# Performance work log

Measured on AMD Instinct MI355X. Metric: run time of the kernel, lower is better.

Reference implementation:

```python
import jax, jax.numpy as jnp
import numpy as np

STRIDE = 1
PAD = 1
K = 3  # kernel is asserted 3x3 in the original module


def _conv2d(x, w, b):
    out = jax.lax.conv_general_dilated(
        x, w, (STRIDE, STRIDE), [(PAD, PAD), (PAD, PAD)],
        dimension_numbers=("NCHW", "OIHW", "NCHW"))
    return out + b[None, :, None, None]


def _bilinear_sample(img, py, px):
    # img: [C, H, W]; py, px: [9, Ho, Wo] float sampling coords.
    # Zero-padded bilinear sampling (matches torchvision deform_conv2d).
    H, W = img.shape[1], img.shape[2]
    y0f = jnp.floor(py)
    x0f = jnp.floor(px)
    ly = py - y0f
    lx = px - x0f
    y0 = y0f.astype(jnp.int32)
    x0 = x0f.astype(jnp.int32)

    def g(yi, xi):
        valid = ((yi >= 0) & (yi < H) & (xi >= 0) & (xi < W)).astype(img.dtype)
        v = img[:, jnp.clip(yi, 0, H - 1), jnp.clip(xi, 0, W - 1)]  # [C,9,Ho,Wo]
        return v * valid[None]

    v00 = g(y0, x0)
    v01 = g(y0, x0 + 1)
    v10 = g(y0 + 1, x0)
    v11 = g(y0 + 1, x0 + 1)
    return (v00 * (1 - ly) * (1 - lx) + v01 * (1 - ly) * lx
            + v10 * ly * (1 - lx) + v11 * ly * lx)  # [C,9,Ho,Wo]


def setup_inputs() -> dict:
    key = jax.random.key(0)
    k1, k2, k3, k4 = jax.random.split(key, 4)
    B, C_in, C_out, H, W = 8, 64, 64, 128, 128
    x = jax.random.normal(k1, (B, C_in, H, W), dtype=jnp.float32)
    # offset predictor params (zero-init in original; small random here so
    # offsets are non-trivial, ~1-2 px)
    offset_w = jax.random.normal(k2, (4, C_in, K, K), dtype=jnp.float32) * 0.05
    offset_b = jax.random.normal(k3, (4,), dtype=jnp.float32) * 0.05
    weight = jax.random.normal(k4, (C_out, C_in, K, K), dtype=jnp.float32)
    return {"x": x, "offset_w": offset_w, "offset_b": offset_b, "weight": weight}


def reference(x, offset_w, offset_b, weight):
    B, C, H, W = x.shape
    o = _conv2d(x, offset_w, offset_b)  # [B, 4, Ho, Wo]
    o_t, o_b, o_l, o_r = o[:, 0], o[:, 1], o[:, 2], o[:, 3]
    z = jnp.zeros_like(o_t)
    # Original builds offset = cat([o_t,0,o_b]*3, [o_l]*3,[0]*3,[o_r]*3) (18 ch)
    # and torchvision reads interleaved (dy_k, dx_k) = (ch[2k], ch[2k+1]).
    # Faithful literal per-kernel-point offsets:
    dy = jnp.stack([o_t, o_b, z, o_t, o_b, o_l, z, z, o_r], axis=1)  # [B,9,Ho,Wo]
    dx = jnp.stack([z, o_t, o_b, z, o_l, o_l, z, o_r, o_r], axis=1)  # [B,9,Ho,Wo]
    Ho, Wo = o.shape[2], o.shape[3]
    ki = jnp.arange(9) // 3
    kj = jnp.arange(9) % 3
    base_y = (jnp.arange(Ho)[None, :, None] * STRIDE - PAD + ki[:, None, None])  # [9,Ho,1]
    base_x = (jnp.arange(Wo)[None, None, :] * STRIDE - PAD + kj[:, None, None])  # [9,1,Wo]
    py = base_y.astype(x.dtype) + dy  # [B,9,Ho,Wo]
    px = base_x.astype(x.dtype) + dx
    sampled = jax.vmap(_bilinear_sample)(x, py, px)  # [B,C,9,Ho,Wo]
    out = jnp.einsum("bckhw,ock->bohw", sampled,
                     weight.reshape(weight.shape[0], C, 9))
    return out
```

## Files before the change

kernel.cpp:

```cpp
#include <hip/hip_runtime.h>

#define H_   128
#define W_   128
#define CIN  64
#define COUT 64
#define B_   8
#define HW_  (H_*W_)

typedef __attribute__((ext_vector_type(8))) short  short8;
typedef __attribute__((ext_vector_type(8))) __bf16 bf16x8;
typedef __attribute__((ext_vector_type(4))) float  f32x4;

__device__ __forceinline__ ushort bf16r(float f) {
    uint u = __builtin_bit_cast(uint, f);
    u += 0x7fff + ((u >> 16) & 1);
    return (ushort)(u >> 16);
}

__global__ void prep_kernel(const float* __restrict__ wt, const float* __restrict__ ow,
                            float* __restrict__ owT, ushort* __restrict__ wTT2)
{
    int idx = blockIdx.x * 256 + threadIdx.x;
    if (idx < 9 * 64 * 64) {
        int kk = idx >> 12;
        int r  = idx & 4095;
        int co = r >> 6, c = r & 63;
        wTT2[idx] = bf16r(wt[(co * 64 + c) * 9 + kk]);
    }
    if (idx < 576 * 4) {
        int ck = idx >> 2, j = idx & 3;
        owT[idx] = ow[j * 576 + ck];
    }
}

__global__ __launch_bounds__(128) void offsets_kernel(
    const float* __restrict__ x, const float* __restrict__ owT,
    const float* __restrict__ ob, float* __restrict__ o)
{
    __shared__ float xs[16][3][132];

    int tid = threadIdx.x;
    int blk = blockIdx.x;
    int b = blk >> 7, h = blk & 127;
    int w = tid;

    for (int i = tid; i < 16 * 3; i += 128) {
        int c = i / 3, r = i - c * 3;
        xs[c][r][0] = 0.f; xs[c][r][1] = 0.f;
        xs[c][r][130] = 0.f; xs[c][r][131] = 0.f;
    }

    float a0 = 0.f, a1 = 0.f, a2 = 0.f, a3 = 0.f;
    const float4* owT4 = (const float4*)owT;

    for (int cc = 0; cc < 4; ++cc) {
        __syncthreads();
        for (int idx = tid; idx < 16 * 3 * 128; idx += 128) {
            int c_l = idx / 384;
            int rem = idx - c_l * 384;
            int row = rem >> 7, ww = rem & 127;
            int gy = h - 1 + row;
            float v = 0.f;
            if ((unsigned)gy < (unsigned)H_)
                v = x[((size_t)(b * CIN + cc * 16 + c_l) * H_ + gy) * W_ + ww];
            xs[c_l][row][ww + 2] = v;
        }
        __syncthreads();
        #pragma unroll
        for (int c_l = 0; c_l < 16; ++c_l) {
            int ckb = (cc * 16 + c_l) * 9;
            #pragma unroll
            for (int ki = 0; ki < 3; ++ki) {
                #pragma unroll
                for (int kj = 0; kj < 3; ++kj) {
                    float v = xs[c_l][ki][w + kj + 1];
                    float4 wv = owT4[ckb + ki * 3 + kj];
                    a0 += v * wv.x; a1 += v * wv.y;
                    a2 += v * wv.z; a3 += v * wv.w;
                }
            }
        }
    }

    size_t base = ((size_t)(b * 4) * H_ + h) * W_ + w;
    o[base]           = a0 + ob[0];
    o[base + HW_]     = a1 + ob[1];
    o[base + 2 * HW_] = a2 + ob[2];
    o[base + 3 * HW_] = a3 + ob[3];
}

__global__ __launch_bounds__(128) void main_kernel(
    const float* __restrict__ x, const float* __restrict__ o,
    const ushort* __restrict__ wTT2, float* __restrict__ out)
{
    __shared__ ushort a_lds[128][72];
    __shared__ ushort w_lds[64][72];

    int tid  = threadIdx.x;
    int blk  = blockIdx.x;
    int b    = blk >> 7, h = blk & 127;
    int w    = tid;
    int lane = tid & 63, wid = tid >> 6;

    size_t obase = ((size_t)(b * 4) * H_ + h) * W_ + w;
    float t  = o[obase];
    float bo = o[obase + HW_];
    float l_ = o[obase + 2 * HW_];
    float r_ = o[obase + 3 * HW_];

    const float* xb = x + ((size_t)b * CIN * HW_);

    f32x4 zero4 = {0.f, 0.f, 0.f, 0.f};
    f32x4 acc[4][4];
    #pragma unroll
    for (int i = 0; i < 4; ++i)
        #pragma unroll
        for (int j = 0; j < 4; ++j) acc[i][j] = zero4;

    for (int cc = 0; cc < 9; ++cc) {
        float dy, dx;
        switch (cc) {
            case 0: dy = t;   dx = 0.f; break;
            case 1: dy = bo;  dx = t;   break;
            case 2: dy = 0.f; dx = bo;  break;
            case 3: dy = t;   dx = 0.f; break;
            case 4: dy = bo;  dx = l_;  break;
            case 5: dy = l_;  dx = l_;  break;
            case 6: dy = 0.f; dx = 0.f; break;
            case 7: dy = 0.f; dx = r_;  break;
            default: dy = r_; dx = r_;  break;
        }
        int ki = cc / 3, kj = cc - ki * 3;
        float py  = (float)(h - 1 + ki) + dy;
        float pxf = (float)(w - 1 + kj) + dx;
        float y0f = floorf(py), x0f = floorf(pxf);
        float ly = py - y0f, lx = pxf - x0f;
        int y0 = (int)y0f, x0 = (int)x0f;
        int y1 = y0 + 1,   x1 = x0 + 1;
        bool vy0 = ((unsigned)y0 < (unsigned)H_);
        bool vy1 = ((unsigned)y1 < (unsigned)H_);
        bool vx0 = ((unsigned)x0 < (unsigned)W_);
        bool vx1 = ((unsigned)x1 < (unsigned)W_);
        int y0c = min(max(y0, 0), H_ - 1), y1c = min(max(y1, 0), H_ - 1);
        int x0c = min(max(x0, 0), W_ - 1), x1c = min(max(x1, 0), W_ - 1);
        int ia0 = y0c * W_ + x0c, ia1 = y0c * W_ + x1c;
        int ia2 = y1c * W_ + x0c, ia3 = y1c * W_ + x1c;
        float omly = 1.f - ly, omlx = 1.f - lx;
        float wt0 = (vy0 && vx0) ? omly * omlx : 0.f;
        float wt1 = (vy0 && vx1) ? omly * lx   : 0.f;
        float wt2 = (vy1 && vx0) ? ly * omlx   : 0.f;
        float wt3 = (vy1 && vx1) ? ly * lx     : 0.f;

        #pragma unroll
        for (int c8 = 0; c8 < 8; ++c8) {
            uint pk[4];
            #pragma unroll
            for (int i2 = 0; i2 < 4; ++i2) {
                const float* xc0 = xb + ((size_t)(c8 * 8 + i2 * 2) << 14);
                const float* xc1 = xb + ((size_t)(c8 * 8 + i2 * 2 + 1) << 14);
                float s0 = wt0 * xc0[ia0] + wt1 * xc0[ia1]
                         + wt2 * xc0[ia2] + wt3 * xc0[ia3];
                float s1 = wt0 * xc1[ia0] + wt1 * xc1[ia1]
                         + wt2 * xc1[ia2] + wt3 * xc1[ia3];
                pk[i2] = (uint)bf16r(s0) | ((uint)bf16r(s1) << 16);
            }
            *(uint4*)&a_lds[tid][c8 * 8] = make_uint4(pk[0], pk[1], pk[2], pk[3]);
        }

        {
            const uint4* src = (const uint4*)(wTT2 + cc * 4096);
            #pragma unroll
            for (int q = 0; q < 4; ++q) {
                int idx = tid + q * 128;
                int co = idx >> 3, c0 = (idx & 7) * 8;
                *(uint4*)&w_lds[co][c0] = src[idx];
            }
        }
        __syncthreads();

        #pragma unroll
        for (int s = 0; s < 2; ++s) {
            int krow = s * 32 + (lane >> 4) * 8;
            bf16x8 af[4];
            #pragma unroll
            for (int i = 0; i < 4; ++i)
                af[i] = __builtin_bit_cast(bf16x8,
                    *(const short8*)&a_lds[wid * 64 + i * 16 + (lane & 15)][krow]);
            #pragma unroll
            for (int j = 0; j < 4; ++j) {
                bf16x8 bf = __builtin_bit_cast(bf16x8,
                    *(const short8*)&w_lds[j * 16 + (lane & 15)][krow]);
                #pragma unroll
                for (int i = 0; i < 4; ++i)
                    acc[i][j] = __builtin_amdgcn_mfma_f32_16x16x32_bf16(
                        af[i], bf, acc[i][j], 0, 0, 0);
            }
        }
        __syncthreads();
    }

    #pragma unroll
    for (int i = 0; i < 4; ++i) {
        int pr = wid * 64 + i * 16 + (lane >> 4) * 4;
        #pragma unroll
        for (int j = 0; j < 4; ++j) {
            int co = j * 16 + (lane & 15);
            *(float4*)&out[((size_t)(b * COUT + co) * H_ + h) * W_ + pr] =
                *(float4*)&acc[i][j];
        }
    }
}

extern "C" void kernel_launch(void* const* d_in, const int* in_sizes, int n_in,
                              void* d_out, int out_size, void* d_ws, size_t ws_size,
                              hipStream_t stream)
{
    const float* x  = (const float*)d_in[0];
    const float* ow = (const float*)d_in[1];
    const float* ob = (const float*)d_in[2];
    const float* wt = (const float*)d_in[3];
    float* out = (float*)d_out;

    float*  o_ws = (float*)d_ws;
    float*  owT  = o_ws + (size_t)B_ * 4 * HW_;
    ushort* wTT2 = (ushort*)(owT + 2304);

    prep_kernel<<<dim3(144), dim3(256), 0, stream>>>(wt, ow, owT, wTT2);
    offsets_kernel<<<dim3(1024), dim3(128), 0, stream>>>(x, owT, ob, o_ws);
    main_kernel<<<dim3(1024), dim3(128), 0, stream>>>(x, o_ws, wTT2, out);
}
```

Measured before the change: 408.3 us.

## Fuse offset conv into main kernel via MFMA, two rows per block

Result: slower. 541.5 us (+32.6%).

```diff
diff --git a/kernel.cpp b/kernel.cpp
--- a/kernel.cpp
+++ b/kernel.cpp
@@ -2,9 +2,6 @@
 
 #define H_   128
 #define W_   128
-#define CIN  64
-#define COUT 64
-#define B_   8
 #define HW_  (H_*W_)
 
 typedef __attribute__((ext_vector_type(8))) short  short8;
@@ -16,168 +13,246 @@
     u += 0x7fff + ((u >> 16) & 1);
     return (ushort)(u >> 16);
 }
+__device__ __forceinline__ float ubf_lo(uint p) {
+    return __builtin_bit_cast(float, p << 16);
+}
+__device__ __forceinline__ float ubf_hi(uint p) {
+    return __builtin_bit_cast(float, p & 0xffff0000u);
+}
 
 __global__ void prep_kernel(const float* __restrict__ wt, const float* __restrict__ ow,
-                            float* __restrict__ owT, ushort* __restrict__ wTT2)
+                            ushort* __restrict__ wB, ushort* __restrict__ owB)
 {
     int idx = blockIdx.x * 256 + threadIdx.x;
     if (idx < 9 * 64 * 64) {
-        int kk = idx >> 12;
-        int r  = idx & 4095;
-        int co = r >> 6, c = r & 63;
-        wTT2[idx] = bf16r(wt[(co * 64 + c) * 9 + kk]);
-    }
-    if (idx < 576 * 4) {
-        int ck = idx >> 2, j = idx & 3;
-        owT[idx] = ow[j * 576 + ck];
-    }
-}
-
-__global__ __launch_bounds__(128) void offsets_kernel(
-    const float* __restrict__ x, const float* __restrict__ owT,
-    const float* __restrict__ ob, float* __restrict__ o)
+        int t  = idx >> 12;
+        int co = (idx >> 6) & 63;
+        int k  = idx & 63;
+        int cc, c;
+        if (t < 8) { cc = k >> 3; c = t * 8 + (k & 7); }
+        else       { cc = 8;      c = k; }
+        wB[idx] = bf16r(wt[(co * 64 + c) * 9 + cc]);
+    }
+    if (idx < 9 * 16 * 64) {
+        int t = idx >> 10;
+        int j = (idx >> 6) & 15;
+        int k = idx & 63;
+        float v = 0.f;
+        if (j < 4) {
+            int cc, c;
+            if (t < 8) { cc = k >> 3; c = t * 8 + (k & 7); }
+            else       { cc = 8;      c = k; }
+            v = ow[(j * 64 + c) * 9 + cc];
+        }
+        owB[idx] = bf16r(v);
+    }
+}
+
+__global__ __launch_bounds__(256, 3) void main_kernel(
+    const float* __restrict__ x, const ushort* __restrict__ wB,
+    const ushort* __restrict__ owB, const float* __restrict__ ob,
+    float* __restrict__ out)
 {
-    __shared__ float xs[16][3][132];
-
-    int tid = threadIdx.x;
-    int blk = blockIdx.x;
-    int b = blk >> 7, h = blk & 127;
-    int w = tid;
-
-    for (int i = tid; i < 16 * 3; i += 128) {
-        int c = i / 3, r = i - c * 3;
-        xs[c][r][0] = 0.f; xs[c][r][1] = 0.f;
-        xs[c][r][130] = 0.f; xs[c][r][131] = 0.f;
-    }
-
-    float a0 = 0.f, a1 = 0.f, a2 = 0.f, a3 = 0.f;
-    const float4* owT4 = (const float4*)owT;
-
-    for (int cc = 0; cc < 4; ++cc) {
-        __syncthreads();
-        for (int idx = tid; idx < 16 * 3 * 128; idx += 128) {
-            int c_l = idx / 384;
-            int rem = idx - c_l * 384;
-            int row = rem >> 7, ww = rem & 127;
-            int gy = h - 1 + row;
-            float v = 0.f;
-            if ((unsigned)gy < (unsigned)H_)
-                v = x[((size_t)(b * CIN + cc * 16 + c_l) * H_ + gy) * W_ + ww];
-            xs[c_l][row][ww + 2] = v;
+    __shared__ __align__(16) ushort a_lds[256][72];
+    __shared__ __align__(16) ushort w_lds[64][72];
+
+    int tid  = threadIdx.x;
+    int blk  = blockIdx.x;
+    int b    = blk & 7;
+    int h0   = (blk >> 3) << 1;
+    int row  = tid >> 7, w = tid & 127;
+    int h    = h0 + row;
+    int lane = tid & 63, wid = tid >> 6;
+
+    const float* xb = x + ((size_t)b << 20);
+
+    f32x4 acc_o[4];
+    #pragma unroll
+    for (int i = 0; i < 4; ++i) acc_o[i] = (f32x4){0.f, 0.f, 0.f, 0.f};
+
+    for (int t = 0; t < 9; ++t) {
+        if (tid < 128) {
+            *(uint4*)&w_lds[tid >> 3][(tid & 7) * 8] =
+                ((const uint4*)(owB + t * 1024))[tid];
+        }
+        if (t < 8) {
+            #pragma unroll
+            for (int cc = 0; cc < 8; ++cc) {
+                int ki = cc / 3, kj = cc - (cc / 3) * 3;
+                int y = h - 1 + ki, xw = w - 1 + kj;
+                bool vv = ((unsigned)y < (unsigned)H_) && ((unsigned)xw < (unsigned)W_);
+                int ia = (y << 7) + xw;
+                uint pk[4];
+                #pragma unroll
+                for (int e = 0; e < 4; ++e) {
+                    const float* p0 = xb + ((size_t)(t * 8 + 2 * e) << 14);
+                    const float* p1 = p0 + 16384;
+                    float s0 = vv ? p0[ia] : 0.f;
+                    float s1 = vv ? p1[ia] : 0.f;
+                    pk[e] = (uint)bf16r(s0) | ((uint)bf16r(s1) << 16);
+                }
+                *(uint4*)&a_lds[tid][cc * 8] = make_uint4(pk[0], pk[1], pk[2], pk[3]);
+            }
+        } else {
+            int y = h + 1, xw = w + 1;
+            bool vv = (y < H_) && (xw < W_);
+            int ia = (y << 7) + xw;
+            #pragma unroll
+            for (int c8 = 0; c8 < 8; ++c8) {
+                uint pk[4];
+                #pragma unroll
+                for (int e = 0; e < 4; ++e) {
+                    const float* p0 = xb + ((size_t)(c8 * 8 + 2 * e) << 14);
+                    const float* p1 = p0 + 16384;
+                    float s0 = vv ? p0[ia] : 0.f;
+                    float s1 = vv ? p1[ia] : 0.f;
+                    pk[e] = (uint)bf16r(s0) | ((uint)bf16r(s1) << 16);
+                }
+                *(uint4*)&a_lds[tid][c8 * 8] = make_uint4(pk[0], pk[1], pk[2], pk[3]);
+            }
         }
         __syncthreads();
         #pragma unroll
-        for (int c_l = 0; c_l < 16; ++c_l) {
-            int ckb = (cc * 16 + c_l) * 9;
-            #pragma unroll
-            for (int ki = 0; ki < 3; ++ki) {
-                #pragma unroll
-                for (int kj = 0; kj < 3; ++kj) {
-                    float v = xs[c_l][ki][w + kj + 1];
-                    float4 wv = owT4[ckb + ki * 3 + kj];
-                    a0 += v * wv.x; a1 += v * wv.y;
-                    a2 += v * wv.z; a3 += v * wv.w;
-                }
-            }
-        }
-    }
-
-    size_t base = ((size_t)(b * 4) * H_ + h) * W_ + w;
-    o[base]           = a0 + ob[0];
-    o[base + HW_]     = a1 + ob[1];
-    o[base + 2 * HW_] = a2 + ob[2];
-    o[base + 3 * HW_] = a3 + ob[3];
-}
-
-__global__ __launch_bounds__(128) void main_kernel(
-    const float* __restrict__ x, const float* __restrict__ o,
-    const ushort* __restrict__ wTT2, float* __restrict__ out)
-{
-    __shared__ ushort a_lds[128][72];
-    __shared__ ushort w_lds[64][72];
-
-    int tid  = threadIdx.x;
-    int blk  = blockIdx.x;
-    int b    = blk >> 7, h = blk & 127;
-    int w    = tid;
-    int lane = tid & 63, wid = tid >> 6;
-
-    size_t obase = ((size_t)(b * 4) * H_ + h) * W_ + w;
-    float t  = o[obase];
-    float bo = o[obase + HW_];
-    float l_ = o[obase + 2 * HW_];
-    float r_ = o[obase + 3 * HW_];
-
-    const float* xb = x + ((size_t)b * CIN * HW_);
-
-    f32x4 zero4 = {0.f, 0.f, 0.f, 0.f};
-    f32x4 acc[4][4];
+        for (int s = 0; s < 2; ++s) {
+            int krow = s * 32 + (lane >> 4) * 8;
+            bf16x8 bfr = __builtin_bit_cast(bf16x8,
+                *(const short8*)&w_lds[lane & 15][krow]);
+            #pragma unroll
+            for (int i = 0; i < 4; ++i) {
+                bf16x8 af = __builtin_bit_cast(bf16x8,
+                    *(const short8*)&a_lds[wid * 64 + i * 16 + (lane & 15)][krow]);
+                acc_o[i] = __builtin_amdgcn_mfma_f32_16x16x32_bf16(af, bfr, acc_o[i], 0, 0, 0);
+            }
+        }
+        __syncthreads();
+    }
+
+    float* o_f = (float*)&w_lds[0][0];
+    {
+        int j4 = lane & 15;
+        if (j4 < 4) {
+            float bias = ob[j4];
+            #pragma unroll
+            for (int i = 0; i < 4; ++i) {
+                int pxb = wid * 64 + i * 16 + ((lane >> 4) << 2);
+                #pragma unroll
+                for (int r = 0; r < 4; ++r)
+                    o_f[j4 * 256 + pxb + r] = acc_o[i][r] + bias;
+            }
+        }
+    }
+    __syncthreads();
+    float t_ = o_f[tid];
+    float bo = o_f[256 + tid];
+    float l_ = o_f[512 + tid];
+    float r_ = o_f[768 + tid];
+
+    uint g_ad[9][4];
+    uint g_wy[9], g_wx[9];
     #pragma unroll
-    for (int i = 0; i < 4; ++i)
-        #pragma unroll
-        for (int j = 0; j < 4; ++j) acc[i][j] = zero4;
-
     for (int cc = 0; cc < 9; ++cc) {
         float dy, dx;
         switch (cc) {
-            case 0: dy = t;   dx = 0.f; break;
-            case 1: dy = bo;  dx = t;   break;
+            case 0: dy = t_;  dx = 0.f; break;
+            case 1: dy = bo;  dx = t_;  break;
             case 2: dy = 0.f; dx = bo;  break;
-            case 3: dy = t;   dx = 0.f; break;
+            case 3: dy = t_;  dx = 0.f; break;
             case 4: dy = bo;  dx = l_;  break;
             case 5: dy = l_;  dx = l_;  break;
             case 6: dy = 0.f; dx = 0.f; break;
             case 7: dy = 0.f; dx = r_;  break;
             default: dy = r_; dx = r_;  break;
         }
-        int ki = cc / 3, kj = cc - ki * 3;
-        float py  = (float)(h - 1 + ki) + dy;
-        float pxf = (float)(w - 1 + kj) + dx;
+        float py  = (float)(h - 1 + cc / 3) + dy;
+        float pxf = (float)(w - 1 + cc - (cc / 3) * 3) + dx;
         float y0f = floorf(py), x0f = floorf(pxf);
         float ly = py - y0f, lx = pxf - x0f;
         int y0 = (int)y0f, x0 = (int)x0f;
         int y1 = y0 + 1,   x1 = x0 + 1;
-        bool vy0 = ((unsigned)y0 < (unsigned)H_);
-        bool vy1 = ((unsigned)y1 < (unsigned)H_);
-        bool vx0 = ((unsigned)x0 < (unsigned)W_);
-        bool vx1 = ((unsigned)x1 < (unsigned)W_);
         int y0c = min(max(y0, 0), H_ - 1), y1c = min(max(y1, 0), H_ - 1);
         int x0c = min(max(x0, 0), W_ - 1), x1c = min(max(x1, 0), W_ - 1);
-        int ia0 = y0c * W_ + x0c, ia1 = y0c * W_ + x1c;
-        int ia2 = y1c * W_ + x0c, ia3 = y1c * W_ + x1c;
-        float omly = 1.f - ly, omlx = 1.f - lx;
-        float wt0 = (vy0 && vx0) ? omly * omlx : 0.f;
-        float wt1 = (vy0 && vx1) ? omly * lx   : 0.f;
-        float wt2 = (vy1 && vx0) ? ly * omlx   : 0.f;
-        float wt3 = (vy1 && vx1) ? ly * lx     : 0.f;
-
+        g_ad[cc][0] = (uint)((((y0c << 7) + x0c) << 2));
+        g_ad[cc][1] = (uint)((((y0c << 7) + x1c) << 2));
+        g_ad[cc][2] = (uint)((((y1c << 7) + x0c) << 2));
+        g_ad[cc][3] = (uint)((((y1c << 7) + x1c) << 2));
+        float ay0 = ((unsigned)y0 < (unsigned)H_) ? 1.f - ly : 0.f;
+        float ay1 = ((unsigned)y1 < (unsigned)H_) ? ly : 0.f;
+        float ax0 = ((unsigned)x0 < (unsigned)W_) ? 1.f - lx : 0.f;
+        float ax1 = ((unsigned)x1 < (unsigned)W_) ? lx : 0.f;
+        g_wy[cc] = (uint)bf16r(ay0) | ((uint)bf16r(ay1) << 16);
+        g_wx[cc] = (uint)bf16r(ax0) | ((uint)bf16r(ax1) << 16);
+    }
+    __syncthreads();
+
+    f32x4 acc[4][4];
+    #pragma unroll
+    for (int i = 0; i < 4; ++i)
         #pragma unroll
-        for (int c8 = 0; c8 < 8; ++c8) {
-            uint pk[4];
-            #pragma unroll
-            for (int i2 = 0; i2 < 4; ++i2) {
-                const float* xc0 = xb + ((size_t)(c8 * 8 + i2 * 2) << 14);
-                const float* xc1 = xb + ((size_t)(c8 * 8 + i2 * 2 + 1) << 14);
-                float s0 = wt0 * xc0[ia0] + wt1 * xc0[ia1]
-                         + wt2 * xc0[ia2] + wt3 * xc0[ia3];
-                float s1 = wt0 * xc1[ia0] + wt1 * xc1[ia1]
-                         + wt2 * xc1[ia2] + wt3 * xc1[ia3];
-                pk[i2] = (uint)bf16r(s0) | ((uint)bf16r(s1) << 16);
-            }
-            *(uint4*)&a_lds[tid][c8 * 8] = make_uint4(pk[0], pk[1], pk[2], pk[3]);
-        }
-
+        for (int j = 0; j < 4; ++j) acc[i][j] = (f32x4){0.f, 0.f, 0.f, 0.f};
+
+    for (int t = 0; t < 9; ++t) {
         {
-            const uint4* src = (const uint4*)(wTT2 + cc * 4096);
-            #pragma unroll
-            for (int q = 0; q < 4; ++q) {
-                int idx = tid + q * 128;
-                int co = idx >> 3, c0 = (idx & 7) * 8;
-                *(uint4*)&w_lds[co][c0] = src[idx];
+            const uint4* src = (const uint4*)(wB + t * 4096);
+            #pragma unroll
+            for (int q = 0; q < 2; ++q) {
+                int i = tid + q * 256;
+                *(uint4*)&w_lds[i >> 3][(i & 7) * 8] = src[i];
+            }
+        }
+        if (t < 8) {
+            #pragma unroll
+            for (int cc = 0; cc < 8; ++cc) {
+                uint a0 = g_ad[cc][0], a1 = g_ad[cc][1];
+                uint a2 = g_ad[cc][2], a3 = g_ad[cc][3];
+                float ay0 = ubf_lo(g_wy[cc]), ay1 = ubf_hi(g_wy[cc]);
+                float ax0 = ubf_lo(g_wx[cc]), ax1 = ubf_hi(g_wx[cc]);
+                float w00 = ay0 * ax0, w01 = ay0 * ax1;
+                float w10 = ay1 * ax0, w11 = ay1 * ax1;
+                uint pk[4];
+                #pragma unroll
+                for (int e = 0; e < 4; ++e) {
+                    const char* p0 = (const char*)(xb + ((size_t)(t * 8 + 2 * e) << 14));
+                    const char* p1 = p0 + 65536;
+                    float s0 = w00 * *(const float*)(p0 + a0)
+                             + w01 * *(const float*)(p0 + a1)
+                             + w10 * *(const float*)(p0 + a2)
+                             + w11 * *(const float*)(p0 + a3);
+                    float s1 = w00 * *(const float*)(p1 + a0)
+                             + w01 * *(const float*)(p1 + a1)
+                             + w10 * *(const float*)(p1 + a2)
+                             + w11 * *(const float*)(p1 + a3);
+                    pk[e] = (uint)bf16r(s0) | ((uint)bf16r(s1) << 16);
+                }
+                *(uint4*)&a_lds[tid][cc * 8] = make_uint4(pk[0], pk[1], pk[2], pk[3]);
+            }
+        } else {
+            uint a0 = g_ad[8][0], a1 = g_ad[8][1];
+            uint a2 = g_ad[8][2], a3 = g_ad[8][3];
+            float ay0 = ubf_lo(g_wy[8]), ay1 = ubf_hi(g_wy[8]);
+            float ax0 = ubf_lo(g_wx[8]), ax1 = ubf_hi(g_wx[8]);
+            float w00 = ay0 * ax0, w01 = ay0 * ax1;
+            float w10 = ay1 * ax0, w11 = ay1 * ax1;
+            #pragma unroll
+            for (int c8 = 0; c8 < 8; ++c8) {
+                uint pk[4];
+                #pragma unroll
+                for (int e = 0; e < 4; ++e) {
+                    const char* p0 = (const char*)(xb + ((size_t)(c8 * 8 + 2 * e) << 14));
+                    const char* p1 = p0 + 65536;
+                    float s0 = w00 * *(const float*)(p0 + a0)
+                             + w01 * *(const float*)(p0 + a1)
+                             + w10 * *(const float*)(p0 + a2)
+                             + w11 * *(const float*)(p0 + a3);
+                    float s1 = w00 * *(const float*)(p1 + a0)
+                             + w01 * *(const float*)(p1 + a1)
+                             + w10 * *(const float*)(p1 + a2)
+                             + w11 * *(const float*)(p1 + a3);
+                    pk[e] = (uint)bf16r(s0) | ((uint)bf16r(s1) << 16);
+                }
+                *(uint4*)&a_lds[tid][c8 * 8] = make_uint4(pk[0], pk[1], pk[2], pk[3]);
             }
         }
         __syncthreads();
-
         #pragma unroll
         for (int s = 0; s < 2; ++s) {
             int krow = s * 32 + (lane >> 4) * 8;
@@ -188,12 +263,12 @@
                     *(const short8*)&a_lds[wid * 64 + i * 16 + (lane & 15)][krow]);
             #pragma unroll
             for (int j = 0; j < 4; ++j) {
-                bf16x8 bf = __builtin_bit_cast(bf16x8,
+                bf16x8 bfr = __builtin_bit_cast(bf16x8,
                     *(const short8*)&w_lds[j * 16 + (lane & 15)][krow]);
                 #pragma unroll
                 for (int i = 0; i < 4; ++i)
                     acc[i][j] = __builtin_amdgcn_mfma_f32_16x16x32_bf16(
-                        af[i], bf, acc[i][j], 0, 0, 0);
+                        af[i], bfr, acc[i][j], 0, 0, 0);
             }
         }
         __syncthreads();
@@ -201,11 +276,13 @@
 
     #pragma unroll
     for (int i = 0; i < 4; ++i) {
-        int pr = wid * 64 + i * 16 + (lane >> 4) * 4;
+        int px = wid * 64 + i * 16 + ((lane >> 4) << 2);
+        int hh = h0 + (px >> 7);
+        int ww = px & 127;
         #pragma unroll
         for (int j = 0; j < 4; ++j) {
             int co = j * 16 + (lane & 15);
-            *(float4*)&out[((size_t)(b * COUT + co) * H_ + h) * W_ + pr] =
+            *(float4*)&out[(((size_t)(b * 64 + co)) * H_ + hh) * W_ + ww] =
                 *(float4*)&acc[i][j];
         }
     }
@@ -221,11 +298,9 @@
     const float* wt = (const float*)d_in[3];
     float* out = (float*)d_out;
 
-    float*  o_ws = (float*)d_ws;
-    float*  owT  = o_ws + (size_t)B_ * 4 * HW_;
-    ushort* wTT2 = (ushort*)(owT + 2304);
-
-    prep_kernel<<<dim3(144), dim3(256), 0, stream>>>(wt, ow, owT, wTT2);
-    offsets_kernel<<<dim3(1024), dim3(128), 0, stream>>>(x, owT, ob, o_ws);
-    main_kernel<<<dim3(1024), dim3(128), 0, stream>>>(x, o_ws, wTT2, out);
-}
+    ushort* wB  = (ushort*)d_ws;
+    ushort* owB = wB + 9 * 64 * 64;
+
+    prep_kernel<<<dim3(144), dim3(256), 0, stream>>>(wt, ow, wB, owB);
+    main_kernel<<<dim3(512), dim3(256), 0, stream>>>(x, wB, owB, ob, out);
+}
```
